# Kernel tuning notes

Hardware: AMD Instinct MI355X
Metric: run time of the kernel (lower is better)

Reference implementation:

```python
import jax, jax.numpy as jnp
import numpy as np
import math

NUM_HEADS = 16
D_MODEL = 1024
D_HEAD = D_MODEL // NUM_HEADS
B, S = 2, 2048


def setup_inputs() -> dict:
    key = jax.random.key(0)
    k1, k2 = jax.random.split(key)
    query = jax.random.normal(k1, (B, S, D_MODEL), dtype=jnp.float32)
    # causal mask: True where masked (j > i)
    mask = jnp.broadcast_to(jnp.triu(jnp.ones((S, S), dtype=bool), k=1), (B, S, S))
    W_o = jax.random.normal(k2, (D_MODEL, D_MODEL), dtype=jnp.float32) * (1.0 / math.sqrt(D_MODEL))
    b_o = jnp.zeros((D_MODEL,), dtype=jnp.float32)
    return {"query": query, "mask": mask, "W_o": W_o, "b_o": b_o}


def reference(query, mask, W_o, b_o):
    # NOTE: faithful to source — q/k/v linear layers are never applied in forward.
    # Self-attention: key = value = query.
    Bq, Sq, D = query.shape
    # split heads: [B, S, D] -> [B, H, S, dh]
    q = query.reshape(Bq, Sq, NUM_HEADS, D_HEAD).transpose(0, 2, 1, 3)
    k = q
    v = q
    # logits: [B, H, Sq, Sk]
    logits = jnp.einsum("bhqd,bhkd->bhqk", q, k) / math.sqrt(D_HEAD)
    logits = jnp.where(mask[:, None, :, :], -jnp.inf, logits)
    attn = jax.nn.softmax(logits, axis=-1)          # [B, H, Sq, Sk]
    out = jnp.einsum("bhqk,bhkd->bhqd", attn, v)    # [B, H, Sq, dh]
    # merge heads: [B, Sq, D]
    out = out.transpose(0, 2, 1, 3).reshape(Bq, Sq, D)
    # output projection (torch Linear: x @ W.T + b)
    return out @ W_o.T + b_o
```

## Files before the change

kernel.cpp:

```cpp
#include <hip/hip_runtime.h>
#include <hip/hip_bf16.h>
#include <stdint.h>

#define SEQ 2048
#define DMODEL 1024

typedef __attribute__((ext_vector_type(8))) short short8;
typedef __attribute__((ext_vector_type(4))) float floatx4;
typedef __fp16 fp16x2 __attribute__((ext_vector_type(2)));
typedef _Float16 half4_t __attribute__((ext_vector_type(4)));

__device__ __forceinline__ floatx4 mfma_bf16_x32(short8 a, short8 b, floatx4 c) {
  return __builtin_amdgcn_mfma_f32_16x16x32_bf16(a, b, c, 0, 0, 0);
}
__device__ __forceinline__ floatx4 mfma_f16_x16(half4_t a, half4_t b, floatx4 c) {
  return __builtin_amdgcn_mfma_f32_16x16x16f16(a, b, c, 0, 0, 0);
}

__device__ __forceinline__ uint16_t f2bf(float x) {
  __hip_bfloat16 h = __float2bfloat16(x);
  return *reinterpret_cast<uint16_t*>(&h);
}
__device__ __forceinline__ float bf2f(uint16_t u) {
  union { uint32_t u; float f; } c; c.u = (uint32_t)u << 16; return c.f;
}
__device__ __forceinline__ uint32_t pk2f16(float a, float b) {
  union { fp16x2 h; uint32_t u; } c;
  c.h = __builtin_amdgcn_cvt_pkrtz(a, b);
  return c.u;
}
__device__ __forceinline__ void glds16(const uint16_t* g, uint16_t* l) {
  __builtin_amdgcn_global_load_lds(
      (const __attribute__((address_space(1))) uint32_t*)g,
      (__attribute__((address_space(3))) uint32_t*)(uint32_t)(uintptr_t)l,
      16, 0, 0);
}

__global__ __launch_bounds__(256) void cvt_kernel(
    const float* __restrict__ q, uint16_t* __restrict__ qbf,
    uint16_t* __restrict__ qf16,
    const float* __restrict__ w, uint16_t* __restrict__ wbf,
    int nq4, int ntot4) {
  int i = blockIdx.x * 256 + threadIdx.x;
  if (i >= ntot4) return;
  if (i < nq4) {
    float4 v = ((const float4*)q)[i];
    ushort4 rb;
    rb.x = f2bf(v.x); rb.y = f2bf(v.y); rb.z = f2bf(v.z); rb.w = f2bf(v.w);
    ((ushort4*)qbf)[i] = rb;
    uint2 hw;
    hw.x = pk2f16(v.x, v.y);
    hw.y = pk2f16(v.z, v.w);
    ((uint2*)qf16)[i] = hw;
  } else {
    int j = i - nq4;
    float4 v = ((const float4*)w)[j];
    ushort4 rb;
    rb.x = f2bf(v.x); rb.y = f2bf(v.y); rb.z = f2bf(v.z); rb.w = f2bf(v.w);
    ((ushort4*)wbf)[j] = rb;
  }
}

__global__ __launch_bounds__(256, 2) void attn_kernel(
    const uint16_t* __restrict__ qbf, const uint16_t* __restrict__ qf16,
    uint16_t* __restrict__ Opart, float* __restrict__ Lpart) {
  const int u    = blockIdx.x >> 5;
  const int seg  = u >> 4;
  const int qt   = ((u >> 3) & 1) ? (u & 7) : (15 - (u & 7));
  const int bh   = blockIdx.x & 31;
  const int b    = bh >> 4;
  const int h    = bh & 15;
  const int tid  = threadIdx.x;
  const int wave = tid >> 6;
  const int lane = tid & 63;
  const int l15  = lane & 15;
  const int quad = lane >> 4;

  __shared__ uint32_t VtU[2][64 * 32];

  const uint16_t* base   = qbf  + (size_t)b * SEQ * DMODEL + h * 64;
  const uint16_t* base16 = qf16 + (size_t)b * SEQ * DMODEL + h * 64;

  short8 qf[2][2];
  #pragma unroll
  for (int s = 0; s < 2; ++s)
    #pragma unroll
    for (int ks = 0; ks < 2; ++ks)
      qf[s][ks] = *(const short8*)(base +
          (size_t)(qt * 128 + s * 64 + wave * 16 + l15) * DMODEL + ks * 32 + quad * 8);

  floatx4 o_acc[2][4];
  float lp[2] = {0.f, 0.f};
  #pragma unroll
  for (int s = 0; s < 2; ++s)
    #pragma unroll
    for (int dt = 0; dt < 4; ++dt) o_acc[s][dt] = (floatx4){0.f, 0.f, 0.f, 0.f};

  const int k0 = (tid >> 3) * 2;
  const int cg = (tid & 7) * 8;
  const int kp_w = (k0 >> 1) & 1;
  const int g4_w = k0 >> 2;

  auto stage = [&](int kt, int buf) {
    const uint16_t* rp = base16 + (size_t)(kt * 64 + k0) * DMODEL + cg;
    uint4 a0 = *(const uint4*)rp;
    uint4 a1 = *(const uint4*)(rp + DMODEL);
    uint16_t e0[8], e1[8];
    *(uint4*)e0 = a0;
    *(uint4*)e1 = a1;
    #pragma unroll
    for (int i2 = 0; i2 < 8; ++i2) {
      int d = cg + i2;
      int p = ((g4_w ^ (d & 15)) + ((d >> 4) << 2)) & 15;
      VtU[buf][d * 32 + p * 2 + kp_w] = (uint32_t)e0[i2] | ((uint32_t)e1[i2] << 16);
    }
  };

  const int lo = seg * (qt + 1);
  const int hi = lo + (qt + 1);
  const int kthi = hi - 1;
  stage(lo, lo & 1);

  auto iter = [&](int kt, int g0m, int g1m, bool d0, bool d1) {
    __syncthreads();
    if (kt < kthi) stage(kt + 1, (kt + 1) & 1);
    const int buf = kt & 1;
    const int gmm = (g0m > g1m) ? g0m : g1m;

    floatx4 sacc[2][4];
    #pragma unroll
    for (int s = 0; s < 2; ++s)
      #pragma unroll
      for (int g = 0; g < 4; ++g) sacc[s][g] = (floatx4){0.f, 0.f, 0.f, 0.f};

    #pragma unroll
    for (int ks = 0; ks < 2; ++ks)
      #pragma unroll
      for (int g = 0; g < 4; ++g)
        if (g <= gmm) {
          short8 kf = *(const short8*)(base +
              (size_t)(kt * 64 + g * 16 + l15) * DMODEL + ks * 32 + quad * 8);
          if (g <= g0m) sacc[0][g] = mfma_bf16_x32(kf, qf[0][ks], sacc[0][g]);
          if (g <= g1m) sacc[1][g] = mfma_bf16_x32(kf, qf[1][ks], sacc[1][g]);
        }

    #pragma unroll
    for (int s = 0; s < 2; ++s) {
      const int gm = s ? g1m : g0m;
      const bool dg = s ? d1 : d0;
      if (gm < 0) continue;
      #pragma unroll
      for (int g = 0; g < 4; ++g)
        if (g <= gm) {
          float pv[4];
          #pragma unroll
          for (int r = 0; r < 4; ++r) {
            float p = __builtin_amdgcn_exp2f(fmaf(sacc[s][g][r], 0.1803369f, -10.f));
            if (dg && g == wave && quad * 4 + r > l15) p = 0.f;
            lp[s] += p;
            pv[r] = p;
          }
          union { half4_t h4; uint32_t u2[2]; } bb;
          bb.u2[0] = pk2f16(pv[0], pv[1]);
          bb.u2[1] = pk2f16(pv[2], pv[3]);
          half4_t bfr = bb.h4;
          #pragma unroll
          for (int dt = 0; dt < 4; ++dt) {
            int d = dt * 16 + l15;
            int p = (((g * 4 + quad) ^ l15) + (dt << 2)) & 15;
            half4_t vf = *(const half4_t*)&VtU[buf][d * 32 + p * 2];
            o_acc[s][dt] = mfma_f16_x16(vf, bfr, o_acc[s][dt]);
          }
        }
    }
  };

  const int dk0 = 2 * qt, dk1 = 2 * qt + 1;
  int kt = lo;
  const int mainEnd = (hi < dk0) ? hi : dk0;
  for (; kt < mainEnd; ++kt) iter(kt, 3, 3, false, false);
  if (kt < hi && kt == dk0) { iter(dk0, wave, 3, true, false); ++kt; }
  if (kt < hi && kt == dk1) { iter(dk1, -1, wave, false, true); }

  const size_t obase = (size_t)seg * (4096 * 1024);
  #pragma unroll
  for (int s = 0; s < 2; ++s) {
    float l = lp[s];
    l += __shfl_xor(l, 16, 64);
    l += __shfl_xor(l, 32, 64);
    int rowg = b * SEQ + qt * 128 + s * 64 + wave * 16 + l15;
    if (quad == 0) Lpart[seg * 65536 + h * 4096 + rowg] = l;
    #pragma unroll
    for (int dt = 0; dt < 4; ++dt) {
      uint16_t ob[4];
      #pragma unroll
      for (int r = 0; r < 4; ++r) ob[r] = f2bf(o_acc[s][dt][r]);
      *(uint2*)&Opart[obase + (size_t)rowg * DMODEL + h * 64 + dt * 16 + quad * 4] =
          *(uint2*)ob;
    }
  }
}

__global__ __launch_bounds__(256) void combine_kernel(
    const uint16_t* __restrict__ Opart, const float* __restrict__ Lpart,
    uint16_t* __restrict__ X) {
  int i = blockIdx.x * 256 + threadIdx.x;
  int row = i >> 7;
  int c8  = (i & 127) * 8;
  int h   = c8 >> 6;
  float inv = 1.0f / (Lpart[h * 4096 + row] + Lpart[65536 + h * 4096 + row]);
  uint16_t a[8], bpt[8], o[8];
  *(uint4*)a   = *(const uint4*)&Opart[(size_t)row * DMODEL + c8];
  *(uint4*)bpt = *(const uint4*)&Opart[(size_t)4096 * 1024 + (size_t)row * DMODEL + c8];
  #pragma unroll
  for (int k = 0; k < 8; ++k)
    o[k] = f2bf((bf2f(a[k]) + bf2f(bpt[k])) * inv);
  *(uint4*)&X[(size_t)row * DMODEL + c8] = *(uint4*)o;
}

__global__ __launch_bounds__(256, 4) void proj_kernel(
    const uint16_t* __restrict__ X, const uint16_t* __restrict__ Wo,
    const float* __restrict__ bo, float* __restrict__ out) {
  const int bx = blockIdx.x;
  const int by = blockIdx.y;
  const int tid = threadIdx.x;
  const int wave = tid >> 6, lane = tid & 63, l15 = lane & 15, quad = lane >> 4;
  const int wr = wave >> 1, wc = wave & 1;

  __shared__ uint16_t As[2][128 * 32];
  __shared__ uint16_t Bs[2][64 * 32];

  floatx4 acc[4][2];
  #pragma unroll
  for (int mt = 0; mt < 4; ++mt)
    #pragma unroll
    for (int nt = 0; nt < 2; ++nt) acc[mt][nt] = (floatx4){0.f, 0.f, 0.f, 0.f};

  const int rw = lane >> 2;
  const int kp = 8 * ((lane & 3) ^ ((lane >> 2) & 3));

  auto stage = [&](int kt, int buf) {
    glds16(X + (size_t)(bx * 128 + wave * 16 + rw) * DMODEL + kt * 32 + kp,
           &As[buf][(wave * 16) * 32 + lane * 8]);
    glds16(X + (size_t)(bx * 128 + 64 + wave * 16 + rw) * DMODEL + kt * 32 + kp,
           &As[buf][(64 + wave * 16) * 32 + lane * 8]);
    glds16(Wo + (size_t)(by * 64 + wave * 16 + rw) * DMODEL + kt * 32 + kp,
           &Bs[buf][(wave * 16) * 32 + lane * 8]);
  };

  stage(0, 0);
  for (int kt = 0; kt < 32; ++kt) {
    __syncthreads();
    if (kt < 31) stage(kt + 1, (kt + 1) & 1);
    const int buf = kt & 1;
    short8 af[4], bf2[2];
    #pragma unroll
    for (int mt = 0; mt < 4; ++mt) {
      int row = wr * 64 + mt * 16 + l15;
      af[mt] = *(const short8*)&As[buf][row * 32 + ((quad ^ (row & 3)) << 3)];
    }
    #pragma unroll
    for (int nt = 0; nt < 2; ++nt) {
      int row = wc * 32 + nt * 16 + l15;
      bf2[nt] = *(const short8*)&Bs[buf][row * 32 + ((quad ^ (row & 3)) << 3)];
    }
    #pragma unroll
    for (int mt = 0; mt < 4; ++mt)
      #pragma unroll
      for (int nt = 0; nt < 2; ++nt)
        acc[mt][nt] = mfma_bf16_x32(af[mt], bf2[nt], acc[mt][nt]);
  }

  #pragma unroll
  for (int nt = 0; nt < 2; ++nt) {
    int colg = by * 64 + wc * 32 + nt * 16 + l15;
    float bias = bo[colg];
    #pragma unroll
    for (int mt = 0; mt < 4; ++mt)
      #pragma unroll
      for (int r2 = 0; r2 < 4; ++r2) {
        int rowg = bx * 128 + wr * 64 + mt * 16 + quad * 4 + r2;
        out[(size_t)rowg * DMODEL + colg] = acc[mt][nt][r2] + bias;
      }
  }
}

extern "C" void kernel_launch(void* const* d_in, const int* in_sizes, int n_in,
                              void* d_out, int out_size, void* d_ws, size_t ws_size,
                              hipStream_t stream) {
  const float* q_f32  = (const float*)d_in[0];
  const float* Wo_f32 = (const float*)d_in[2];
  const float* bo     = (const float*)d_in[3];
  float* out = (float*)d_out;

  uint16_t* qbf   = (uint16_t*)d_ws;
  uint16_t* X     = (uint16_t*)((char*)d_ws + (size_t)8 * 1024 * 1024);
  uint16_t* wobf  = (uint16_t*)((char*)d_ws + (size_t)16 * 1024 * 1024);
  uint16_t* Opart = (uint16_t*)((char*)d_ws + (size_t)18 * 1024 * 1024);
  float*    Lpart = (float*)((char*)d_ws + (size_t)34 * 1024 * 1024);
  uint16_t* qf16  = (uint16_t*)((char*)d_ws + (size_t)35 * 1024 * 1024);

  const int nq4 = 2 * SEQ * DMODEL / 4;
  const int nw4 = DMODEL * DMODEL / 4;
  const int nt4 = nq4 + nw4;
  cvt_kernel<<<dim3((nt4 + 255) / 256), dim3(256), 0, stream>>>(
      q_f32, qbf, qf16, Wo_f32, wobf, nq4, nt4);

  attn_kernel<<<dim3(1024), dim3(256), 0, stream>>>(qbf, qf16, Opart, Lpart);
  combine_kernel<<<dim3(2048), dim3(256), 0, stream>>>(Opart, Lpart, X);
  proj_kernel<<<dim3(32, 16), dim3(256), 0, stream>>>(X, wobf, bo, out);
}
```

Measured before the change: 166.0 us.

## Pretranspose V into global fp16 layout and drop LDS staging in attention

Adds a transpose kernel that writes V as a head-major, d-by-seq fp16 array. The attention kernel now reads V fragments straight from global memory instead of staging and transposing them in shared memory with a barrier every iteration. The P·V loop is reordered so each V fragment is shared by both query sub-tiles, and the block-to-tile mapping pairs the two segments of a query tile next to each other. The trade is an extra kernel launch and more global and L2 traffic for V reads, in exchange for no LDS use and no per-iteration synchronisation.

```diff
diff --git a/kernel.cpp b/kernel.cpp
--- a/kernel.cpp
+++ b/kernel.cpp
@@ -37,36 +37,62 @@
 }
 
 __global__ __launch_bounds__(256) void cvt_kernel(
-    const float* __restrict__ q, uint16_t* __restrict__ qbf,
-    uint16_t* __restrict__ qf16,
-    const float* __restrict__ w, uint16_t* __restrict__ wbf,
+    const float* __restrict__ q, uint16_t* __restrict__ qd,
+    const float* __restrict__ w, uint16_t* __restrict__ wd,
     int nq4, int ntot4) {
   int i = blockIdx.x * 256 + threadIdx.x;
   if (i >= ntot4) return;
-  if (i < nq4) {
-    float4 v = ((const float4*)q)[i];
-    ushort4 rb;
-    rb.x = f2bf(v.x); rb.y = f2bf(v.y); rb.z = f2bf(v.z); rb.w = f2bf(v.w);
-    ((ushort4*)qbf)[i] = rb;
-    uint2 hw;
-    hw.x = pk2f16(v.x, v.y);
-    hw.y = pk2f16(v.z, v.w);
-    ((uint2*)qf16)[i] = hw;
-  } else {
-    int j = i - nq4;
-    float4 v = ((const float4*)w)[j];
-    ushort4 rb;
-    rb.x = f2bf(v.x); rb.y = f2bf(v.y); rb.z = f2bf(v.z); rb.w = f2bf(v.w);
-    ((ushort4*)wbf)[j] = rb;
+  const float* src = (i < nq4) ? q : w;
+  uint16_t* dst = (i < nq4) ? qd : wd;
+  int j = (i < nq4) ? i : i - nq4;
+  float4 v = ((const float4*)src)[j];
+  ushort4 r;
+  r.x = f2bf(v.x); r.y = f2bf(v.y); r.z = f2bf(v.z); r.w = f2bf(v.w);
+  ((ushort4*)dst)[j] = r;
+}
+
+__global__ __launch_bounds__(256) void transpose_kernel(
+    const float* __restrict__ q, uint16_t* __restrict__ VtG) {
+  const int bh = blockIdx.x & 31;
+  const int kt = blockIdx.x >> 5;
+  const int b = bh >> 4, h = bh & 15;
+  const int t = threadIdx.x;
+  __shared__ uint16_t tile[64][65];
+  {
+    const int key = t & 63;
+    const int dh = (t >> 6) * 16;
+    const float* src = q + (size_t)(b * SEQ + kt * 64 + key) * DMODEL + h * 64 + dh;
+    #pragma unroll
+    for (int i = 0; i < 4; ++i) {
+      float4 v = *(const float4*)(src + i * 4);
+      uint32_t p0 = pk2f16(v.x, v.y);
+      uint32_t p1 = pk2f16(v.z, v.w);
+      tile[key][dh + i * 4 + 0] = (uint16_t)p0;
+      tile[key][dh + i * 4 + 1] = (uint16_t)(p0 >> 16);
+      tile[key][dh + i * 4 + 2] = (uint16_t)p1;
+      tile[key][dh + i * 4 + 3] = (uint16_t)(p1 >> 16);
+    }
+  }
+  __syncthreads();
+  {
+    const int d = t >> 2;
+    const int kq = (t & 3) * 16;
+    uint16_t buf[16];
+    #pragma unroll
+    for (int i = 0; i < 16; ++i) buf[i] = tile[kq + i][d];
+    uint16_t* dst = &VtG[((size_t)bh * 64 + d) * SEQ + kt * 64 + kq];
+    *(uint4*)dst       = *(uint4*)&buf[0];
+    *(uint4*)(dst + 8) = *(uint4*)&buf[8];
   }
 }
 
 __global__ __launch_bounds__(256, 2) void attn_kernel(
-    const uint16_t* __restrict__ qbf, const uint16_t* __restrict__ qf16,
+    const uint16_t* __restrict__ qbf, const uint16_t* __restrict__ VtG,
     uint16_t* __restrict__ Opart, float* __restrict__ Lpart) {
   const int u    = blockIdx.x >> 5;
-  const int seg  = u >> 4;
-  const int qt   = ((u >> 3) & 1) ? (u & 7) : (15 - (u & 7));
+  const int pair = u >> 1;
+  const int seg  = u & 1;
+  const int qt   = (pair < 8) ? 15 - pair : pair - 8;
   const int bh   = blockIdx.x & 31;
   const int b    = bh >> 4;
   const int h    = bh & 15;
@@ -76,10 +102,8 @@
   const int l15  = lane & 15;
   const int quad = lane >> 4;
 
-  __shared__ uint32_t VtU[2][64 * 32];
-
-  const uint16_t* base   = qbf  + (size_t)b * SEQ * DMODEL + h * 64;
-  const uint16_t* base16 = qf16 + (size_t)b * SEQ * DMODEL + h * 64;
+  const uint16_t* base  = qbf + (size_t)b * SEQ * DMODEL + h * 64;
+  const uint16_t* vbase = VtG + (size_t)bh * 64 * SEQ;
 
   short8 qf[2][2];
   #pragma unroll
@@ -96,35 +120,10 @@
     #pragma unroll
     for (int dt = 0; dt < 4; ++dt) o_acc[s][dt] = (floatx4){0.f, 0.f, 0.f, 0.f};
 
-  const int k0 = (tid >> 3) * 2;
-  const int cg = (tid & 7) * 8;
-  const int kp_w = (k0 >> 1) & 1;
-  const int g4_w = k0 >> 2;
-
-  auto stage = [&](int kt, int buf) {
-    const uint16_t* rp = base16 + (size_t)(kt * 64 + k0) * DMODEL + cg;
-    uint4 a0 = *(const uint4*)rp;
-    uint4 a1 = *(const uint4*)(rp + DMODEL);
-    uint16_t e0[8], e1[8];
-    *(uint4*)e0 = a0;
-    *(uint4*)e1 = a1;
-    #pragma unroll
-    for (int i2 = 0; i2 < 8; ++i2) {
-      int d = cg + i2;
-      int p = ((g4_w ^ (d & 15)) + ((d >> 4) << 2)) & 15;
-      VtU[buf][d * 32 + p * 2 + kp_w] = (uint32_t)e0[i2] | ((uint32_t)e1[i2] << 16);
-    }
-  };
-
   const int lo = seg * (qt + 1);
   const int hi = lo + (qt + 1);
-  const int kthi = hi - 1;
-  stage(lo, lo & 1);
 
   auto iter = [&](int kt, int g0m, int g1m, bool d0, bool d1) {
-    __syncthreads();
-    if (kt < kthi) stage(kt + 1, (kt + 1) & 1);
-    const int buf = kt & 1;
     const int gmm = (g0m > g1m) ? g0m : g1m;
 
     floatx4 sacc[2][4];
@@ -145,13 +144,14 @@
         }
 
     #pragma unroll
-    for (int s = 0; s < 2; ++s) {
-      const int gm = s ? g1m : g0m;
-      const bool dg = s ? d1 : d0;
-      if (gm < 0) continue;
-      #pragma unroll
-      for (int g = 0; g < 4; ++g)
-        if (g <= gm) {
+    for (int g = 0; g < 4; ++g)
+      if (g <= gmm) {
+        half4_t pb[2];
+        const bool act0 = (g <= g0m), act1 = (g <= g1m);
+        #pragma unroll
+        for (int s = 0; s < 2; ++s) {
+          if (!(s ? act1 : act0)) continue;
+          const bool dg = s ? d1 : d0;
           float pv[4];
           #pragma unroll
           for (int r = 0; r < 4; ++r) {
@@ -163,16 +163,16 @@
           union { half4_t h4; uint32_t u2[2]; } bb;
           bb.u2[0] = pk2f16(pv[0], pv[1]);
           bb.u2[1] = pk2f16(pv[2], pv[3]);
-          half4_t bfr = bb.h4;
-          #pragma unroll
-          for (int dt = 0; dt < 4; ++dt) {
-            int d = dt * 16 + l15;
-            int p = (((g * 4 + quad) ^ l15) + (dt << 2)) & 15;
-            half4_t vf = *(const half4_t*)&VtU[buf][d * 32 + p * 2];
-            o_acc[s][dt] = mfma_f16_x16(vf, bfr, o_acc[s][dt]);
-          }
+          pb[s] = bb.h4;
         }
-    }
+        #pragma unroll
+        for (int dt = 0; dt < 4; ++dt) {
+          half4_t vf = *(const half4_t*)(vbase +
+              (size_t)(dt * 16 + l15) * SEQ + kt * 64 + g * 16 + quad * 4);
+          if (act0) o_acc[0][dt] = mfma_f16_x16(vf, pb[0], o_acc[0][dt]);
+          if (act1) o_acc[1][dt] = mfma_f16_x16(vf, pb[1], o_acc[1][dt]);
+        }
+      }
   };
 
   const int dk0 = 2 * qt, dk1 = 2 * qt + 1;
@@ -298,15 +298,16 @@
   uint16_t* wobf  = (uint16_t*)((char*)d_ws + (size_t)16 * 1024 * 1024);
   uint16_t* Opart = (uint16_t*)((char*)d_ws + (size_t)18 * 1024 * 1024);
   float*    Lpart = (float*)((char*)d_ws + (size_t)34 * 1024 * 1024);
-  uint16_t* qf16  = (uint16_t*)((char*)d_ws + (size_t)35 * 1024 * 1024);
+  uint16_t* VtG   = (uint16_t*)((char*)d_ws + (size_t)35 * 1024 * 1024);
 
   const int nq4 = 2 * SEQ * DMODEL / 4;
   const int nw4 = DMODEL * DMODEL / 4;
   const int nt4 = nq4 + nw4;
   cvt_kernel<<<dim3((nt4 + 255) / 256), dim3(256), 0, stream>>>(
-      q_f32, qbf, qf16, Wo_f32, wobf, nq4, nt4);
-
-  attn_kernel<<<dim3(1024), dim3(256), 0, stream>>>(qbf, qf16, Opart, Lpart);
+      q_f32, qbf, Wo_f32, wobf, nq4, nt4);
+  transpose_kernel<<<dim3(1024), dim3(256), 0, stream>>>(q_f32, VtG);
+
+  attn_kernel<<<dim3(1024), dim3(256), 0, stream>>>(qbf, VtG, Opart, Lpart);
   combine_kernel<<<dim3(2048), dim3(256), 0, stream>>>(Opart, Lpart, X);
   proj_kernel<<<dim3(32, 16), dim3(256), 0, stream>>>(X, wobf, bo, out);
 }
```

Result: slower. 215.7 us (+29.9%).
